# Kernel tuning notes

Hardware: AMD Instinct MI355X
Metric: run time of the kernel (lower is better)

## Reference

```python
import jax, jax.numpy as jnp
import numpy as np

N_SENS, N_HID, N_MOT = 10000, 400000, 1000
E_SH, E_HH, E_HM = 4_000_000, 16_000_000, 400_000
BETA, THR, SLOPE = 0.9, 1.0, 25.0  # snn.Leaky(beta, threshold), surrogate.fast_sigmoid(slope=25)

# Heaviside spike with fast-sigmoid surrogate gradient (matches snnTorch)
@jax.custom_vjp
def spike(x):
    return (x > 0).astype(x.dtype)

def _spike_fwd(x):
    return (x > 0).astype(x.dtype), x

def _spike_bwd(x, g):
    return (g / (SLOPE * jnp.abs(x) + 1.0) ** 2,)

spike.defvjp(_spike_fwd, _spike_bwd)

def lif(inp, mem):
    # snn.Leaky, reset_mechanism='zero': mem = beta*mem + I; spike; reset to 0 where spiked
    mem = BETA * mem + inp
    spk = spike(mem - THR)
    mem = mem - jax.lax.stop_gradient(spk) * mem  # reset detached, as in snnTorch
    return spk, mem

def spmm_t(pre_idx, post_idx, w, pre_spikes, n_post):
    # torch.sparse.mm(W^T, pre_spikes): gather pre activity along edges, scatter-add to post
    contrib = w * pre_spikes[pre_idx]          # [E]
    return jax.ops.segment_sum(contrib, post_idx, num_segments=n_post)

def setup_inputs() -> dict:
    key = jax.random.key(0)
    ks = jax.random.split(key, 16)
    std_sh = 1.0 / np.sqrt(N_SENS * 0.001)
    std_hh = 1.0 / np.sqrt(N_HID * 0.0001)
    std_hm = 1.0 / np.sqrt(N_HID * 0.001)
    return {
        "sensory_input": jax.random.uniform(ks[0], (N_SENS,), jnp.float32),
        "sensory_mem": jax.random.uniform(ks[1], (N_SENS,), jnp.float32),
        "hidden_mem": jax.random.uniform(ks[2], (N_HID,), jnp.float32),
        "motor_mem": jax.random.uniform(ks[3], (N_MOT,), jnp.float32),
        "hidden_prev_spikes": (jax.random.uniform(ks[4], (N_HID,)) < 0.05).astype(jnp.float32),
        "w_sh": jax.random.normal(ks[5], (E_SH,), jnp.float32) * std_sh,
        "w_hh": jax.random.normal(ks[6], (E_HH,), jnp.float32) * std_hh,
        "w_hm": jax.random.normal(ks[7], (E_HM,), jnp.float32) * std_hm,
        "sh_pre": jax.random.randint(ks[8], (E_SH,), 0, N_SENS, jnp.int32),
        "sh_post": jax.random.randint(ks[9], (E_SH,), 0, N_HID, jnp.int32),
        "hh_pre": jax.random.randint(ks[10], (E_HH,), 0, N_HID, jnp.int32),
        "hh_post": jax.random.randint(ks[11], (E_HH,), 0, N_HID, jnp.int32),
        "hm_pre": jax.random.randint(ks[12], (E_HM,), 0, N_HID, jnp.int32),
        "hm_post": jax.random.randint(ks[13], (E_HM,), 0, N_MOT, jnp.int32),
    }

def reference(sensory_input, sensory_mem, hidden_mem, motor_mem, hidden_prev_spikes,
              w_sh, w_hh, w_hm, sh_pre, sh_post, hh_pre, hh_post, hm_pre, hm_post):
    sens_spk, _ = lif(sensory_input * 5.0, sensory_mem)
    hid_in = spmm_t(sh_pre, sh_post, w_sh, sens_spk, N_HID)
    hid_in = hid_in + 0.5 * spmm_t(hh_pre, hh_post, w_hh, hidden_prev_spikes, N_HID)
    hid_spk, _ = lif(hid_in * 5.0, hidden_mem)
    mot_in = spmm_t(hm_pre, hm_post, w_hm, hid_spk, N_MOT)
    mot_spk, _ = lif(mot_in * 20.0, motor_mem)
    return mot_spk
```

## Files before the change

### kernel.cpp

```cpp
#include <hip/hip_runtime.h>


#define N_SENS 10000
#define N_HID  400000
#define N_MOT  1000

#define CHUNK_LOG 14
#define CHUNK     (1 << CHUNK_LOG)
#define NBUCKET   25
#define CAP       196608
#define NCOPY     10

#define SENS_MW   320
#define HID_MW    12512

#define G_SH      2
#define BUF_SH    8192
#define G_HH      8
#define BUF_HH    2048

#define SMEM_BYTES 66816

#define NB_HM     64

__global__ void make_masks(const float* __restrict__ sens_in,
                           const float* __restrict__ sens_mem,
                           const float* __restrict__ hid_prev,
                           uint2* __restrict__ smask,
                           uint2* __restrict__ hmask,
                           float* __restrict__ extra,
                           int* __restrict__ cursors, int nb_sens) {
    bool pred = false;
    int i;
    uint2* dst;
    int maxw;
    if ((int)blockIdx.x < nb_sens) {
        if (blockIdx.x == 0 && threadIdx.x < 32) cursors[threadIdx.x] = 0;
        i = blockIdx.x * blockDim.x + threadIdx.x;
        if (i < N_SENS) pred = (0.9f * sens_mem[i] + 5.0f * sens_in[i]) > 1.0f;
        dst = smask; maxw = SENS_MW / 2;
    } else {
        i = (blockIdx.x - nb_sens) * blockDim.x + threadIdx.x;
        if (i < N_HID) { pred = (hid_prev[i] != 0.0f); extra[i] = 0.0f; }
        dst = hmask; maxw = HID_MW / 2;
    }
    unsigned long long b = __ballot(pred);
    if ((threadIdx.x & 63) == 0) {
        int w = i >> 6;
        if (w < maxw) dst[w] = make_uint2((unsigned)b, (unsigned)(b >> 32));
    }
}

template <int G, int BUFCAP>
__device__ __forceinline__
void bin_body(const int* __restrict__ pre, const int* __restrict__ post,
              const float* __restrict__ w, int n_e, float scale,
              const unsigned* sm, uint2* buf, int (*h)[32], int* total,
              float* __restrict__ extra, int blockStart) {
    const int tid = threadIdx.x;
    const int lane = tid & 63;
    const unsigned long long lt = (1ull << lane) - 1ull;
    const int rep = (tid >> 6) & 3;
    const int base4 = (blockStart >> 2) + tid;
    #pragma unroll
    for (int g = 0; g < G; ++g) {
        int e4 = base4 + g * 1024;
        int e0 = e4 << 2;
        int4 pr4 = make_int4(-1, -1, -1, -1);
        int4 po4 = make_int4(0, 0, 0, 0);
        float4 wv4 = make_float4(0.f, 0.f, 0.f, 0.f);
        if (e0 + 3 < n_e) {
            pr4 = ((const int4*)pre)[e4];
            po4 = ((const int4*)post)[e4];
            wv4 = ((const float4*)w)[e4];
        } else if (e0 < n_e) {
            int t[4] = {-1, -1, -1, -1}, q[4] = {0, 0, 0, 0};
            float f[4] = {0.f, 0.f, 0.f, 0.f};
            for (int k = 0; k < 4; ++k) {
                int e = e0 + k;
                if (e < n_e) { t[k] = pre[e]; q[k] = post[e]; f[k] = w[e]; }
            }
            pr4 = make_int4(t[0], t[1], t[2], t[3]);
            po4 = make_int4(q[0], q[1], q[2], q[3]);
            wv4 = make_float4(f[0], f[1], f[2], f[3]);
        }
        int   prk[4] = {pr4.x, pr4.y, pr4.z, pr4.w};
        int   pok[4] = {po4.x, po4.y, po4.z, po4.w};
        float wk[4]  = {wv4.x, wv4.y, wv4.z, wv4.w};
        #pragma unroll
        for (int k = 0; k < 4; ++k) {
            int pr = prk[k];
            bool act = (pr >= 0) && ((sm[pr >> 5] >> (pr & 31)) & 1u);
            unsigned long long m = __ballot(act);
            if (!m) continue;
            int bse = 0;
            if (lane == 0) bse = atomicAdd(total, (int)__popcll(m));
            bse = __shfl(bse, 0);
            if (act) {
                int idx = bse + (int)__popcll(m & lt);
                unsigned p = (unsigned)pok[k];
                float wv = scale * wk[k];
                if (idx < BUFCAP) {
                    buf[idx] = make_uint2(p, __float_as_uint(wv));
                    atomicAdd(&h[rep][p >> CHUNK_LOG], 1);
                } else {
                    atomicAdd(&extra[p], wv);
                }
            }
        }
    }
}

__global__ __launch_bounds__(1024, 8)
void bin_stream(const int* __restrict__ sh_pre, const int* __restrict__ sh_post,
                const float* __restrict__ w_sh, const unsigned* __restrict__ smask,
                int e_sh, int nb_sh,
                const int* __restrict__ hh_pre, const int* __restrict__ hh_post,
                const float* __restrict__ w_hh, const unsigned* __restrict__ hmask,
                int e_hh, int nb_hh,
                uint2* __restrict__ pairs, int* __restrict__ gcursor,
                float* __restrict__ extra) {
    __shared__ __align__(16) char smem[SMEM_BYTES];
    __shared__ int h[4][32];
    __shared__ int gb[32];
    __shared__ int lcur[32];
    __shared__ int total;

    const int tid = threadIdx.x;
    const int bid = blockIdx.x;

    int nmin = (nb_sh < nb_hh) ? nb_sh : nb_hh;
    bool is_sh;
    int idx;
    if (bid < 2 * nmin) { is_sh = ((bid & 1) == 0); idx = bid >> 1; }
    else { is_sh = (nb_sh > nb_hh); idx = bid - 2 * nmin + nmin; }

    const unsigned* gm = is_sh ? smask : hmask;
    const int mw = is_sh ? SENS_MW : HID_MW;
    unsigned* sm = (unsigned*)smem;
    uint2* buf = (uint2*)(smem + (size_t)mw * 4);

    if (tid < 128) ((int*)h)[tid] = 0;
    if (tid == 0) total = 0;
    for (int i = tid; i < mw / 4; i += 1024)
        ((uint4*)sm)[i] = ((const uint4*)gm)[i];
    __syncthreads();

    if (is_sh)
        bin_body<G_SH, BUF_SH>(sh_pre, sh_post, w_sh, e_sh, 1.0f,
                               sm, buf, h, &total, extra, idx * (4096 * G_SH));
    else
        bin_body<G_HH, BUF_HH>(hh_pre, hh_post, w_hh, e_hh, 0.5f,
                               sm, buf, h, &total, extra, idx * (4096 * G_HH));
    __syncthreads();

    int bufcap = is_sh ? BUF_SH : BUF_HH;
    int tot = total; if (tot > bufcap) tot = bufcap;

    if (tid < NBUCKET) {
        int hb = h[0][tid] + h[1][tid] + h[2][tid] + h[3][tid];
        gb[tid] = hb ? atomicAdd(&gcursor[tid], hb) : 0;
        lcur[tid] = 0;
    }
    __syncthreads();

    for (int k = tid; k < tot; k += 1024) {
        uint2 u = buf[k];
        int b = u.x >> CHUNK_LOG;
        int s = atomicAdd(&lcur[b], 1);
        int pos = gb[b] + s;
        if (pos < CAP)
            pairs[(size_t)b * CAP + pos] =
                make_uint2(u.x & (CHUNK - 1), u.y);
        else
            atomicAdd(&extra[u.x], __uint_as_float(u.y));
    }
}

__global__ __launch_bounds__(1024, 8)
void accum_bucket(const uint2* __restrict__ pairs,
                  const int* __restrict__ cursors,
                  float* __restrict__ partials) {
    int bucket = blockIdx.x / NCOPY;
    int copy   = blockIdx.x % NCOPY;
    __shared__ float acc[CHUNK];
    for (int i = threadIdx.x; i < CHUNK; i += blockDim.x) acc[i] = 0.0f;
    __syncthreads();

    int count = cursors[bucket];
    if (count > CAP) count = CAP;
    int begin = (int)((long long)count * copy / NCOPY);
    int end   = (int)((long long)count * (copy + 1) / NCOPY);
    const uint2* src = pairs + (size_t)bucket * CAP;
    for (int i = begin + threadIdx.x; i < end; i += blockDim.x) {
        uint2 u = src[i];
        atomicAdd(&acc[u.x], __uint_as_float(u.y));
    }
    __syncthreads();
    float* dst = partials + ((size_t)bucket * NCOPY + copy) * CHUNK;
    for (int i = threadIdx.x; i < CHUNK; i += blockDim.x) dst[i] = acc[i];
}

__global__ void reduce_lif_hidden_mask(const float* __restrict__ partials,
                                       const float* __restrict__ extra,
                                       const float* __restrict__ mem,
                                       uint2* __restrict__ mask) {
    int i = blockIdx.x * blockDim.x + threadIdx.x;
    bool pred = false;
    if (i < N_HID) {
        int b = i >> CHUNK_LOG, local = i & (CHUNK - 1);
        const float* p = partials + (size_t)b * NCOPY * CHUNK + local;
        float sum = extra[i];
        #pragma unroll
        for (int c = 0; c < NCOPY; ++c) sum += p[(size_t)c * CHUNK];
        pred = (0.9f * mem[i] + 5.0f * sum) > 1.0f;
    }
    unsigned long long bal = __ballot(pred);
    if ((threadIdx.x & 63) == 0) {
        int w = i >> 6;
        if (w < HID_MW / 2)
            mask[w] = make_uint2((unsigned)bal, (unsigned)(bal >> 32));
    }
}

__global__ __launch_bounds__(1024, 8)
void scatter_motor_mask(const int* __restrict__ pre,
                        const int* __restrict__ post,
                        const float* __restrict__ w,
                        const unsigned* __restrict__ gmask,
                        float* __restrict__ partials, int n_edges) {
    __shared__ float acc[N_MOT];
    __shared__ unsigned sm[HID_MW];
    for (int i = threadIdx.x; i < HID_MW / 4; i += blockDim.x)
        ((uint4*)sm)[i] = ((const uint4*)gmask)[i];
    for (int j = threadIdx.x; j < N_MOT; j += blockDim.x) acc[j] = 0.0f;
    __syncthreads();
    for (int e = blockIdx.x * blockDim.x + threadIdx.x; e < n_edges;
         e += gridDim.x * blockDim.x) {
        int pr = pre[e];
        if ((sm[pr >> 5] >> (pr & 31)) & 1u)
            atomicAdd(&acc[post[e]], w[e]);
    }
    __syncthreads();
    float* out = partials + (size_t)blockIdx.x * N_MOT;
    for (int j = threadIdx.x; j < N_MOT; j += blockDim.x) out[j] = acc[j];
}

__global__ void reduce_lif_motor(const float* __restrict__ partials, int nb,
                                 const float* __restrict__ mem,
                                 float* __restrict__ out) {
    int m = blockIdx.x * blockDim.x + threadIdx.x;
    if (m >= N_MOT) return;
    float sum = 0.0f;
    for (int b = 0; b < nb; ++b) sum += partials[(size_t)b * N_MOT + m];
    float v = 0.9f * mem[m] + 20.0f * sum;
    out[m] = (v > 1.0f) ? 1.0f : 0.0f;
}

__global__ void lif_kernel(const float* __restrict__ inp,
                           const float* __restrict__ mem_in,
                           float* __restrict__ spk,
                           float scale, int n) {
    int i = blockIdx.x * blockDim.x + threadIdx.x;
    if (i < n) {
        float m = 0.9f * mem_in[i] + scale * inp[i];
        spk[i] = (m > 1.0f) ? 1.0f : 0.0f;
    }
}

__global__ void scatter_dev(const int* __restrict__ pre,
                            const int* __restrict__ post,
                            const float* __restrict__ w,
                            const float* __restrict__ spikes,
                            float* __restrict__ out,
                            float scale, int n_edges) {
    int e = blockIdx.x * blockDim.x + threadIdx.x;
    if (e >= n_edges) return;
    float s = spikes[pre[e]];
    if (s != 0.0f) atomicAdd(&out[post[e]], scale * w[e] * s);
}

__global__ void lif_hidden_direct(const float* __restrict__ hid_in,
                                  const float* __restrict__ mem,
                                  float* __restrict__ spk) {
    int i = blockIdx.x * blockDim.x + threadIdx.x;
    if (i >= N_HID) return;
    float m = 0.9f * mem[i] + 5.0f * hid_in[i];
    spk[i] = (m > 1.0f) ? 1.0f : 0.0f;
}

__global__ void scatter_motor_f(const int* __restrict__ pre,
                                const int* __restrict__ post,
                                const float* __restrict__ w,
                                const float* __restrict__ spikes,
                                float* __restrict__ partials, int n_edges) {
    __shared__ float acc[N_MOT];
    for (int j = threadIdx.x; j < N_MOT; j += blockDim.x) acc[j] = 0.0f;
    __syncthreads();
    for (int e = blockIdx.x * blockDim.x + threadIdx.x; e < n_edges;
         e += gridDim.x * blockDim.x) {
        float s = spikes[pre[e]];
        if (s != 0.0f) atomicAdd(&acc[post[e]], w[e] * s);
    }
    __syncthreads();
    float* out = partials + (size_t)blockIdx.x * N_MOT;
    for (int j = threadIdx.x; j < N_MOT; j += blockDim.x) out[j] = acc[j];
}

extern "C" void kernel_launch(void* const* d_in, const int* in_sizes, int n_in,
                              void* d_out, int out_size, void* d_ws, size_t ws_size,
                              hipStream_t stream) {
    const float* sensory_input = (const float*)d_in[0];
    const float* sensory_mem   = (const float*)d_in[1];
    const float* hidden_mem    = (const float*)d_in[2];
    const float* motor_mem     = (const float*)d_in[3];
    const float* hidden_prev   = (const float*)d_in[4];
    const float* w_sh          = (const float*)d_in[5];
    const float* w_hh          = (const float*)d_in[6];
    const float* w_hm          = (const float*)d_in[7];
    const int*   sh_pre        = (const int*)d_in[8];
    const int*   sh_post       = (const int*)d_in[9];
    const int*   hh_pre        = (const int*)d_in[10];
    const int*   hh_post       = (const int*)d_in[11];
    const int*   hm_pre        = (const int*)d_in[12];
    const int*   hm_post       = (const int*)d_in[13];
    const int e_sh = in_sizes[5];
    const int e_hh = in_sizes[6];
    const int e_hm = in_sizes[7];
    const int B = 256;

    size_t o_cursor = 0;
    size_t o_extra  = 32;
    size_t o_pairs  = o_extra + N_HID;
    size_t o_part   = o_pairs + (size_t)NBUCKET * CAP * 2;
    size_t o_smask  = o_part + (size_t)NBUCKET * NCOPY * CHUNK;
    size_t o_hmaskp = o_smask + SENS_MW;
    size_t o_hmasks = o_hmaskp + HID_MW;
    size_t o_mpart  = o_hmasks + HID_MW;
    size_t f_need   = o_mpart + (size_t)NB_HM * N_MOT;
    bool fast = (ws_size / sizeof(float)) >= f_need;

    float* ws = (float*)d_ws;
    if (fast) {
        int*      cursors = (int*)(ws + o_cursor);
        float*    extra   = ws + o_extra;
        uint2*    pairs   = (uint2*)(ws + o_pairs);
        float*    part    = ws + o_part;
        unsigned* smask   = (unsigned*)(ws + o_smask);
        unsigned* hmaskp  = (unsigned*)(ws + o_hmaskp);
        unsigned* hmasks  = (unsigned*)(ws + o_hmasks);
        float*    mpart   = ws + o_mpart;

        int nb_sens = (N_SENS + B - 1) / B;
        int nb_hidm = (N_HID + B - 1) / B;
        make_masks<<<nb_sens + nb_hidm, B, 0, stream>>>(
            sensory_input, sensory_mem, hidden_prev,
            (uint2*)smask, (uint2*)hmaskp, extra, cursors, nb_sens);

        int nb_sh = (e_sh + 4096 * G_SH - 1) / (4096 * G_SH);
        int nb_hh = (e_hh + 4096 * G_HH - 1) / (4096 * G_HH);
        bin_stream<<<nb_sh + nb_hh, 1024, 0, stream>>>(
            sh_pre, sh_post, w_sh, smask, e_sh, nb_sh,
            hh_pre, hh_post, w_hh, hmaskp, e_hh, nb_hh,
            pairs, cursors, extra);

        accum_bucket<<<NBUCKET * NCOPY, 1024, 0, stream>>>(pairs, cursors, part);
        reduce_lif_hidden_mask<<<(N_HID + B - 1) / B, B, 0, stream>>>(
            part, extra, hidden_mem, (uint2*)hmasks);
        scatter_motor_mask<<<NB_HM, 1024, 0, stream>>>(
            hm_pre, hm_post, w_hm, hmasks, mpart, e_hm);
        reduce_lif_motor<<<(N_MOT + B - 1) / B, B, 0, stream>>>(
            mpart, NB_HM, motor_mem, (float*)d_out);
    } else {
        float* hid_in   = ws;
        float* sens_spk = hid_in + N_HID;
        float* hid_spk  = sens_spk + 10016;
        float* mpart    = hid_spk + N_HID;
        hipMemsetAsync(hid_in, 0, (size_t)N_HID * sizeof(float), stream);
        lif_kernel<<<(N_SENS + B - 1) / B, B, 0, stream>>>(
            sensory_input, sensory_mem, sens_spk, 5.0f, N_SENS);
        scatter_dev<<<(e_sh + B - 1) / B, B, 0, stream>>>(
            sh_pre, sh_post, w_sh, sens_spk, hid_in, 1.0f, e_sh);
        scatter_dev<<<(e_hh + B - 1) / B, B, 0, stream>>>(
            hh_pre, hh_post, w_hh, hidden_prev, hid_in, 0.5f, e_hh);
        lif_hidden_direct<<<(N_HID + B - 1) / B, B, 0, stream>>>(
            hid_in, hidden_mem, hid_spk);
        scatter_motor_f<<<NB_HM, B, 0, stream>>>(
            hm_pre, hm_post, w_hm, hid_spk, mpart, e_hm);
        reduce_lif_motor<<<(N_MOT + B - 1) / B, B, 0, stream>>>(
            mpart, NB_HM, motor_mem, (float*)d_out);
    }
}
```

Before: 326.8 us.

## Use per-wave shared segments instead of block-wide atomic cursor; split bin kernels

Each wave now compacts its active edges into its own fixed shared-memory segment with a register-held count, which removes the per-ballot shared atomic on a block-wide total and the shuffle that followed it. The combined sensory/hidden binning kernel is split into two specialized kernels, each sizing its shared memory for its own mask. The aim is less atomic contention and smaller static LDS per kernel, at the cost of two launches that now run one after the other instead of interleaved. The per-wave caps (512 and 128 entries) could overflow more often than the old block-wide buffer, sending more entries to global atomics on extra.

```diff
diff --git a/kernel.cpp b/kernel.cpp
--- a/kernel.cpp
+++ b/kernel.cpp
@@ -15,11 +15,11 @@
 #define HID_MW    12512
 
 #define G_SH      2
-#define BUF_SH    8192
+#define SEG_SH    512
 #define G_HH      8
-#define BUF_HH    2048
-
-#define SMEM_BYTES 66816
+#define SEG_HH    128
+
+#define NWAVE     16
 
 #define NB_HM     64
 
@@ -51,16 +51,20 @@
     }
 }
 
-template <int G, int BUFCAP>
+template <int G, int SEG>
 __device__ __forceinline__
 void bin_body(const int* __restrict__ pre, const int* __restrict__ post,
               const float* __restrict__ w, int n_e, float scale,
-              const unsigned* sm, uint2* buf, int (*h)[32], int* total,
+              const unsigned* sm, uint2* buf, int (*h)[32], int* wcnt,
               float* __restrict__ extra, int blockStart) {
     const int tid = threadIdx.x;
     const int lane = tid & 63;
+    const int wid = tid >> 6;
     const unsigned long long lt = (1ull << lane) - 1ull;
-    const int rep = (tid >> 6) & 3;
+    const int rep = wid & 3;
+    const int segbase = wid * SEG;
+    int wcount = 0;
+
     const int base4 = (blockStart >> 2) + tid;
     #pragma unroll
     for (int g = 0; g < G; ++g) {
@@ -74,15 +78,14 @@
             po4 = ((const int4*)post)[e4];
             wv4 = ((const float4*)w)[e4];
         } else if (e0 < n_e) {
-            int t[4] = {-1, -1, -1, -1}, q[4] = {0, 0, 0, 0};
-            float f[4] = {0.f, 0.f, 0.f, 0.f};
-            for (int k = 0; k < 4; ++k) {
-                int e = e0 + k;
-                if (e < n_e) { t[k] = pre[e]; q[k] = post[e]; f[k] = w[e]; }
+            for (int kk = 0; kk < 4; ++kk) {
+                int e = e0 + kk;
+                if (e < n_e) {
+                    ((int*)&pr4)[kk] = pre[e];
+                    ((int*)&po4)[kk] = post[e];
+                    ((float*)&wv4)[kk] = w[e];
+                }
             }
-            pr4 = make_int4(t[0], t[1], t[2], t[3]);
-            po4 = make_int4(q[0], q[1], q[2], q[3]);
-            wv4 = make_float4(f[0], f[1], f[2], f[3]);
         }
         int   prk[4] = {pr4.x, pr4.y, pr4.z, pr4.w};
         int   pok[4] = {po4.x, po4.y, po4.z, po4.w};
@@ -92,89 +95,93 @@
             int pr = prk[k];
             bool act = (pr >= 0) && ((sm[pr >> 5] >> (pr & 31)) & 1u);
             unsigned long long m = __ballot(act);
-            if (!m) continue;
-            int bse = 0;
-            if (lane == 0) bse = atomicAdd(total, (int)__popcll(m));
-            bse = __shfl(bse, 0);
             if (act) {
-                int idx = bse + (int)__popcll(m & lt);
+                int idx = wcount + (int)__popcll(m & lt);
                 unsigned p = (unsigned)pok[k];
                 float wv = scale * wk[k];
-                if (idx < BUFCAP) {
-                    buf[idx] = make_uint2(p, __float_as_uint(wv));
+                if (idx < SEG) {
+                    buf[segbase + idx] = make_uint2(p, __float_as_uint(wv));
                     atomicAdd(&h[rep][p >> CHUNK_LOG], 1);
                 } else {
                     atomicAdd(&extra[p], wv);
                 }
             }
+            wcount += (int)__popcll(m);
         }
     }
-}
-
-__global__ __launch_bounds__(1024, 8)
-void bin_stream(const int* __restrict__ sh_pre, const int* __restrict__ sh_post,
-                const float* __restrict__ w_sh, const unsigned* __restrict__ smask,
-                int e_sh, int nb_sh,
-                const int* __restrict__ hh_pre, const int* __restrict__ hh_post,
-                const float* __restrict__ w_hh, const unsigned* __restrict__ hmask,
-                int e_hh, int nb_hh,
-                uint2* __restrict__ pairs, int* __restrict__ gcursor,
-                float* __restrict__ extra) {
-    __shared__ __align__(16) char smem[SMEM_BYTES];
-    __shared__ int h[4][32];
-    __shared__ int gb[32];
-    __shared__ int lcur[32];
-    __shared__ int total;
-
+    if (lane == 0) wcnt[wid] = (wcount < SEG) ? wcount : SEG;
+}
+
+template <int SEG>
+__device__ __forceinline__
+void bin_flush(uint2* buf, int (*h)[32], int* wcnt, int* gb, int* lcur,
+               uint2* __restrict__ pairs, int* __restrict__ gcursor,
+               float* __restrict__ extra) {
     const int tid = threadIdx.x;
-    const int bid = blockIdx.x;
-
-    int nmin = (nb_sh < nb_hh) ? nb_sh : nb_hh;
-    bool is_sh;
-    int idx;
-    if (bid < 2 * nmin) { is_sh = ((bid & 1) == 0); idx = bid >> 1; }
-    else { is_sh = (nb_sh > nb_hh); idx = bid - 2 * nmin + nmin; }
-
-    const unsigned* gm = is_sh ? smask : hmask;
-    const int mw = is_sh ? SENS_MW : HID_MW;
-    unsigned* sm = (unsigned*)smem;
-    uint2* buf = (uint2*)(smem + (size_t)mw * 4);
-
-    if (tid < 128) ((int*)h)[tid] = 0;
-    if (tid == 0) total = 0;
-    for (int i = tid; i < mw / 4; i += 1024)
-        ((uint4*)sm)[i] = ((const uint4*)gm)[i];
-    __syncthreads();
-
-    if (is_sh)
-        bin_body<G_SH, BUF_SH>(sh_pre, sh_post, w_sh, e_sh, 1.0f,
-                               sm, buf, h, &total, extra, idx * (4096 * G_SH));
-    else
-        bin_body<G_HH, BUF_HH>(hh_pre, hh_post, w_hh, e_hh, 0.5f,
-                               sm, buf, h, &total, extra, idx * (4096 * G_HH));
-    __syncthreads();
-
-    int bufcap = is_sh ? BUF_SH : BUF_HH;
-    int tot = total; if (tot > bufcap) tot = bufcap;
-
     if (tid < NBUCKET) {
         int hb = h[0][tid] + h[1][tid] + h[2][tid] + h[3][tid];
         gb[tid] = hb ? atomicAdd(&gcursor[tid], hb) : 0;
         lcur[tid] = 0;
     }
     __syncthreads();
-
-    for (int k = tid; k < tot; k += 1024) {
-        uint2 u = buf[k];
-        int b = u.x >> CHUNK_LOG;
-        int s = atomicAdd(&lcur[b], 1);
-        int pos = gb[b] + s;
-        if (pos < CAP)
-            pairs[(size_t)b * CAP + pos] =
-                make_uint2(u.x & (CHUNK - 1), u.y);
-        else
-            atomicAdd(&extra[u.x], __uint_as_float(u.y));
-    }
+    for (int s = 0; s < NWAVE; ++s) {
+        int tot = wcnt[s];
+        for (int k = tid; k < tot; k += 1024) {
+            uint2 u = buf[s * SEG + k];
+            int b = u.x >> CHUNK_LOG;
+            int sl = atomicAdd(&lcur[b], 1);
+            int pos = gb[b] + sl;
+            if (pos < CAP)
+                pairs[(size_t)b * CAP + pos] =
+                    make_uint2(u.x & (CHUNK - 1), u.y);
+            else
+                atomicAdd(&extra[u.x], __uint_as_float(u.y));
+        }
+    }
+}
+
+__global__ __launch_bounds__(1024, 8)
+void bin_sh_k(const int* __restrict__ pre, const int* __restrict__ post,
+              const float* __restrict__ w, const unsigned* __restrict__ gmask,
+              int n_e, uint2* __restrict__ pairs, int* __restrict__ gcursor,
+              float* __restrict__ extra) {
+    __shared__ unsigned sm[SENS_MW];
+    __shared__ uint2 buf[NWAVE * SEG_SH];
+    __shared__ int h[4][32];
+    __shared__ int wcnt[NWAVE];
+    __shared__ int gb[32];
+    __shared__ int lcur[32];
+    const int tid = threadIdx.x;
+    for (int i = tid; i < SENS_MW / 4; i += 1024)
+        ((uint4*)sm)[i] = ((const uint4*)gmask)[i];
+    if (tid < 128) ((int*)h)[tid] = 0;
+    __syncthreads();
+    bin_body<G_SH, SEG_SH>(pre, post, w, n_e, 1.0f, sm, buf, h, wcnt,
+                           extra, blockIdx.x * (4096 * G_SH));
+    __syncthreads();
+    bin_flush<SEG_SH>(buf, h, wcnt, gb, lcur, pairs, gcursor, extra);
+}
+
+__global__ __launch_bounds__(1024, 8)
+void bin_hh_k(const int* __restrict__ pre, const int* __restrict__ post,
+              const float* __restrict__ w, const unsigned* __restrict__ gmask,
+              int n_e, uint2* __restrict__ pairs, int* __restrict__ gcursor,
+              float* __restrict__ extra) {
+    __shared__ unsigned sm[HID_MW];
+    __shared__ uint2 buf[NWAVE * SEG_HH];
+    __shared__ int h[4][32];
+    __shared__ int wcnt[NWAVE];
+    __shared__ int gb[32];
+    __shared__ int lcur[32];
+    const int tid = threadIdx.x;
+    for (int i = tid; i < HID_MW / 4; i += 1024)
+        ((uint4*)sm)[i] = ((const uint4*)gmask)[i];
+    if (tid < 128) ((int*)h)[tid] = 0;
+    __syncthreads();
+    bin_body<G_HH, SEG_HH>(pre, post, w, n_e, 0.5f, sm, buf, h, wcnt,
+                           extra, blockIdx.x * (4096 * G_HH));
+    __syncthreads();
+    bin_flush<SEG_HH>(buf, h, wcnt, gb, lcur, pairs, gcursor, extra);
 }
 
 __global__ __launch_bounds__(1024, 8)
@@ -357,12 +364,12 @@
             sensory_input, sensory_mem, hidden_prev,
             (uint2*)smask, (uint2*)hmaskp, extra, cursors, nb_sens);
 
+        int nb_hh = (e_hh + 4096 * G_HH - 1) / (4096 * G_HH);
         int nb_sh = (e_sh + 4096 * G_SH - 1) / (4096 * G_SH);
-        int nb_hh = (e_hh + 4096 * G_HH - 1) / (4096 * G_HH);
-        bin_stream<<<nb_sh + nb_hh, 1024, 0, stream>>>(
-            sh_pre, sh_post, w_sh, smask, e_sh, nb_sh,
-            hh_pre, hh_post, w_hh, hmaskp, e_hh, nb_hh,
-            pairs, cursors, extra);
+        bin_hh_k<<<nb_hh, 1024, 0, stream>>>(
+            hh_pre, hh_post, w_hh, hmaskp, e_hh, pairs, cursors, extra);
+        bin_sh_k<<<nb_sh, 1024, 0, stream>>>(
+            sh_pre, sh_post, w_sh, smask, e_sh, pairs, cursors, extra);
 
         accum_bucket<<<NBUCKET * NCOPY, 1024, 0, stream>>>(pairs, cursors, part);
         reduce_lif_hidden_mask<<<(N_HID + B - 1) / B, B, 0, stream>>>(
```

New measurement: 331.5 us. About the same (+1.5%).
